# Optimization experiments

Measured on AMD Instinct MI355X. Metric: run time of the kernel, lower is better.

The kernel has to match this reference:

```python
import jax, jax.numpy as jnp
import numpy as np

N_HEAD = 8
D_HEAD = 64  # emb_size == d_model // n_head


def _proj(x, w):
    # x: (B, 1, d_model, max_len), w: (n_head*emb_size, 1, 25, 1) -> conv VALID
    y = jax.lax.conv_general_dilated(
        x, w, window_strides=(1, 1), padding='VALID',
        dimension_numbers=('NCHW', 'OIHW', 'NCHW'))  # (B, C, H1, L)
    B, C, H1, L = y.shape
    y = y.reshape(B, C, H1 // N_HEAD, N_HEAD, L).mean(axis=3)  # (B, C, H2, L)
    # view(B, -1, n_head, d_head).transpose(1, 2) -> (B, n_head, S, d_head)
    y = y.reshape(B, -1, N_HEAD, D_HEAD).transpose(0, 2, 1, 3)
    return y


def setup_inputs() -> dict:
    key = jax.random.key(0)
    ks = jax.random.split(key, 7)
    B, d_model, max_len = 8, 512, 16
    C = N_HEAD * D_HEAD  # 512
    return {
        'query': jax.random.normal(ks[0], (B, 1, d_model, max_len), jnp.float32),
        'key':   jax.random.normal(ks[1], (B, 1, d_model, max_len), jnp.float32),
        'value': jax.random.normal(ks[2], (B, 1, d_model, max_len), jnp.float32),
        'wq': jax.random.normal(ks[3], (C, 1, 25, 1), jnp.float32) * 0.1,
        'wk': jax.random.normal(ks[4], (C, 1, 25, 1), jnp.float32) * 0.1,
        'wv': jax.random.normal(ks[5], (C, 1, 25, 1), jnp.float32) * 0.1,
        'w_out': jax.random.normal(ks[6], (1, 1, 1, 1), jnp.float32),
        'b_out': jnp.zeros((1,), jnp.float32),
    }


def reference(query, key, value, wq, wk, wv, w_out, b_out):
    q = _proj(query, wq)   # (B, H, S, Dh)
    k = _proj(key, wk)
    v = _proj(value, wv)
    scale = 1.0 / jnp.sqrt(jnp.asarray(D_HEAD, q.dtype))
    scores = jnp.einsum('bhqd,bhkd->bhqk', q, k) * scale
    attn = jax.nn.softmax(scores, axis=-1)  # dropout is identity in eval
    x = jnp.einsum('bhqk,bhkd->bhqd', attn, v)
    B = x.shape[0]
    x = x.transpose(0, 2, 1, 3).reshape(B, -1, N_HEAD * D_HEAD)  # (B, S, d_model)
    # conv_out: 1x1 Conv2d(1,1) == scalar scale + bias
    x = x * w_out.reshape(()) + b_out.reshape(())
    return x, attn
```

## Files before the change

kernel.cpp:

```cpp
#include <hip/hip_runtime.h>
#include <hip/hip_bf16.h>
#include <cstdint>
#include <cstddef>

#define B_    8
#define H_    8
#define BH_   64
#define S_    976
#define SP_   992
#define D_    64
#define DM_   512
#define L_    16
#define H2_   61
#define KW_   25
#define EFF_  32
#define XOFF  3997696
#define OSTR  68
#define PWC   132

typedef __attribute__((ext_vector_type(8))) short bf16x8;
typedef __attribute__((ext_vector_type(4))) short bf16x4;
typedef __attribute__((ext_vector_type(4))) unsigned short u16x4;
typedef __attribute__((ext_vector_type(4))) float f32x4;

__device__ __forceinline__ unsigned short f2bfu(float f) {
    union { float f; unsigned u; } v; v.f = f;
    unsigned u = v.u;
    u += 0x7fffu + ((u >> 16) & 1u);
    return (unsigned short)(u >> 16);
}
__device__ __forceinline__ unsigned packbf(float a, float b) {
    return (unsigned)f2bfu(a) | ((unsigned)f2bfu(b) << 16);
}
__device__ __forceinline__ float bflo(unsigned u) {
    union { unsigned u; float f; } v; v.u = u << 16; return v.f;
}
__device__ __forceinline__ float bfhi(unsigned u) {
    union { unsigned u; float f; } v; v.u = u & 0xffff0000u; return v.f;
}

__device__ __forceinline__ f32x4 mfma16(bf16x4 a, bf16x4 b, f32x4 c) {
#if __has_builtin(__builtin_amdgcn_mfma_f32_16x16x16bf16_1k)
    return __builtin_amdgcn_mfma_f32_16x16x16bf16_1k(a, b, c, 0, 0, 0);
#else
    asm volatile("v_mfma_f32_16x16x16_bf16 %0, %1, %2, %0"
                 : "+v"(c) : "v"(a), "v"(b));
    return c;
#endif
}

__global__ __launch_bounds__(256) void proj_kernel(
    const float* __restrict__ qin, const float* __restrict__ kin,
    const float* __restrict__ vin, const float* __restrict__ wq,
    const float* __restrict__ wk, const float* __restrict__ wv,
    short* __restrict__ qws, short* __restrict__ kws, short* __restrict__ vtws) {
    __shared__ float xl[536 * L_];
    __shared__ float wl[32 * 32];
    int blk = blockIdx.x;
    int cg  = blk & 15;
    int b   = (blk >> 4) & 7;
    int tz  = blk >> 7;
    const float* x    = (tz == 0) ? qin : (tz == 1) ? kin : vin;
    const float* wsrc = (tz == 0) ? wq  : (tz == 1) ? wk  : wv;

    const float4* xb4 = (const float4*)(x + b * DM_ * L_);
    float4* xl4 = (float4*)xl;
    for (int i = threadIdx.x; i < DM_ * L_ / 4; i += 256) xl4[i] = xb4[i];
    for (int i = DM_ * L_ + threadIdx.x; i < 536 * L_; i += 256) xl[i] = 0.f;

    for (int i = threadIdx.x; i < 1024; i += 256) {
        int ci = i >> 5;
        int t  = i & 31;
        int c  = cg * 32 + ci;
        int jlo = (t - 24 > 0) ? t - 24 : 0;
        int jhi = (t < 7) ? t : 7;
        float s = 0.f;
        for (int jj = jlo; jj <= jhi; ++jj) s += wsrc[c * KW_ + (t - jj)];
        wl[i] = s * 0.125f;
    }
    __syncthreads();

    int c_local = threadIdx.x >> 3;
    int slot    = threadIdx.x & 7;
    int c       = cg * 32 + c_local;
    float wreg[EFF_];
    #pragma unroll
    for (int i = 0; i < EFF_; ++i) wreg[i] = wl[c_local * 32 + i];

    for (int it = 0; it < 8; ++it) {
        int pt  = slot + it * 8;
        int h2b = pt >> 2;
        int l0  = (pt & 3) * 4;
        float acc[4][4];
        #pragma unroll
        for (int d = 0; d < 4; ++d)
            #pragma unroll
            for (int jj = 0; jj < 4; ++jj) acc[d][jj] = 0.f;
        const float* xp = &xl[(h2b * 32) * L_ + l0];
        #pragma unroll
        for (int k = 0; k < 56; ++k) {
            float4 xv = *(const float4*)(xp + k * L_);
            #pragma unroll
            for (int d = 0; d < 4; ++d) {
                int t = k - 8 * d;
                if (t >= 0 && t < EFF_) {
                    acc[d][0] = fmaf(xv.x, wreg[t], acc[d][0]);
                    acc[d][1] = fmaf(xv.y, wreg[t], acc[d][1]);
                    acc[d][2] = fmaf(xv.z, wreg[t], acc[d][2]);
                    acc[d][3] = fmaf(xv.w, wreg[t], acc[d][3]);
                }
            }
        }
        #pragma unroll
        for (int d = 0; d < 4; ++d) {
            int h2 = h2b * 4 + d;
            if (h2 < H2_) {
                int f0   = c * S_ + h2 * L_ + l0;
                int s    = f0 >> 9;
                int head = (f0 >> 6) & 7;
                int dh   = f0 & 63;
                int bh   = b * H_ + head;
                if (tz == 2) {
                    #pragma unroll
                    for (int jj = 0; jj < 4; ++jj)
                        vtws[((size_t)bh * D_ + dh + jj) * SP_ + s] =
                            (short)f2bfu(acc[d][jj]);
                } else {
                    u16x4 u = { f2bfu(acc[d][0]), f2bfu(acc[d][1]),
                                f2bfu(acc[d][2]), f2bfu(acc[d][3]) };
                    short* dst = (tz == 0) ? qws : kws;
                    *(u16x4*)(void*)&dst[((size_t)bh * S_ + s) * D_ + dh] = u;
                }
            }
        }
    }
}

__global__ __launch_bounds__(256) void attn_kernel(
    const short* __restrict__ qws, const short* __restrict__ kws,
    const short* __restrict__ vtws, const float* __restrict__ w_out,
    const float* __restrict__ b_out, float* __restrict__ out) {
    __shared__ unsigned pw[4][16][PWC];
    __shared__ float sums[4][16];

    int w    = threadIdx.x >> 6;
    int lane = threadIdx.x & 63;
    int l16  = lane & 15;
    int g    = lane >> 4;

    int blk = blockIdx.x;
    int xcd = blk & 7;
    int j   = blk >> 3;
    int bh  = xcd + 8 * (j / H2_);
    int qt  = j % H2_;
    int s0  = qt * 16;

    int t0 = (w == 0) ? 0 : 16 + (w - 1) * 15;
    int nt = (w == 0) ? 16 : 15;

    const short* qb = qws + ((size_t)bh * S_ + s0 + l16) * D_ + g * 8;
    bf16x8 q0 = *(const bf16x8*)qb;
    bf16x8 q1 = *(const bf16x8*)(qb + 32);
    const short* kbase = kws + ((size_t)bh * S_ + l16) * D_ + g * 8;
    const short* vbase = vtws + ((size_t)bh * D_ + l16) * SP_ + g * 4;

    f32x4 o0 = {0.f,0.f,0.f,0.f}, o1 = {0.f,0.f,0.f,0.f};
    f32x4 o2 = {0.f,0.f,0.f,0.f}, o3 = {0.f,0.f,0.f,0.f};
    float sa = 0.f, sb = 0.f, sc_ = 0.f, sd = 0.f;

    #pragma unroll
    for (int ct = 0; ct < 16; ++ct) {
        if (ct < nt) {
            int gt = t0 + ct;
            const short* kb = kbase + (size_t)gt * 16 * D_;
            bf16x8 k0 = *(const bf16x8*)kb;
            bf16x8 k1 = *(const bf16x8*)(kb + 32);
            const short* vb = vbase + gt * 16;
            bf16x4 v0 = *(const bf16x4*)(vb);
            bf16x4 v1 = *(const bf16x4*)(vb + 16 * SP_);
            bf16x4 v2 = *(const bf16x4*)(vb + 32 * SP_);
            bf16x4 v3 = *(const bf16x4*)(vb + 48 * SP_);
            f32x4 acc = {0.f, 0.f, 0.f, 0.f};
            acc = __builtin_amdgcn_mfma_f32_16x16x32_bf16(k0, q0, acc, 0, 0, 0);
            acc = __builtin_amdgcn_mfma_f32_16x16x32_bf16(k1, q1, acc, 0, 0, 0);
            float e0 = __expf(acc[0] * 0.125f);
            float e1 = __expf(acc[1] * 0.125f);
            float e2 = __expf(acc[2] * 0.125f);
            float e3 = __expf(acc[3] * 0.125f);
            sa += e0; sb += e1; sc_ += e2; sd += e3;
            unsigned u0 = packbf(e0, e1);
            unsigned u1 = packbf(e2, e3);
            uint2 pk2 = {u0, u1};
            *(uint2*)(void*)&pw[w][l16][ct * 8 + g * 2] = pk2;
            union { uint2 u; bf16x4 v; } pc;
            pc.u.x = u0; pc.u.y = u1;
            o0 = mfma16(pc.v, v0, o0);
            o1 = mfma16(pc.v, v1, o1);
            o2 = mfma16(pc.v, v2, o2);
            o3 = mfma16(pc.v, v3, o3);
        }
    }
    float sum = (sa + sb) + (sc_ + sd);
    sum += __shfl_xor(sum, 16);
    sum += __shfl_xor(sum, 32);
    if (lane < 16) sums[w][l16] = sum;
    __syncthreads();

    {
        int colbase = t0 * 16;
        bool act = lane < nt * 4;
        float* abase = out + XOFF + ((size_t)bh * S_ + s0) * S_ + colbase + lane * 4;
        #pragma unroll
        for (int r = 0; r < 16; ++r) {
            float invr = 1.f / ((sums[0][r] + sums[1][r]) +
                                (sums[2][r] + sums[3][r]));
            if (act) {
                uint2 raw = *(const uint2*)(void*)&pw[w][r][lane * 2];
                f32x4 pv = { bflo(raw.x) * invr, bfhi(raw.x) * invr,
                             bflo(raw.y) * invr, bfhi(raw.y) * invr };
                __builtin_nontemporal_store(pv, (f32x4*)(abase + (size_t)r * S_));
            }
        }
    }
    __syncthreads();

    float* olds = (float*)&pw[0][0][0];
    {
        float* ob = olds + w * 16 * OSTR;
        #pragma unroll
        for (int i = 0; i < 4; ++i) {
            int q = g * 4 + i;
            ob[q * OSTR +  0 + l16] = o0[i];
            ob[q * OSTR + 16 + l16] = o1[i];
            ob[q * OSTR + 32 + l16] = o2[i];
            ob[q * OSTR + 48 + l16] = o3[i];
        }
    }
    __syncthreads();

    {
        float wo = w_out[0], bo = b_out[0];
        int b = bh >> 3, hh = bh & 7;
        #pragma unroll
        for (int rr = 0; rr < 4; ++rr) {
            int r = w * 4 + rr;
            float invr = 1.f / ((sums[0][r] + sums[1][r]) +
                                (sums[2][r] + sums[3][r]));
            float s1 = invr * wo;
            int o = r * OSTR + lane;
            float v = olds[o] + olds[16*OSTR + o] + olds[32*OSTR + o] +
                      olds[48*OSTR + o];
            out[((size_t)b * S_ + s0 + r) * DM_ + hh * D_ + lane] = v * s1 + bo;
        }
    }
}

extern "C" void kernel_launch(void* const* d_in, const int* in_sizes, int n_in,
                              void* d_out, int out_size, void* d_ws, size_t ws_size,
                              hipStream_t stream) {
    const float* q   = (const float*)d_in[0];
    const float* k   = (const float*)d_in[1];
    const float* v   = (const float*)d_in[2];
    const float* wq  = (const float*)d_in[3];
    const float* wk  = (const float*)d_in[4];
    const float* wv  = (const float*)d_in[5];
    const float* wo  = (const float*)d_in[6];
    const float* bo  = (const float*)d_in[7];

    char* ws = (char*)d_ws;
    short* qws  = (short*)(ws + 196608);
    short* kws  = qws + (size_t)BH_ * S_ * D_;
    short* vtws = kws + (size_t)BH_ * S_ * D_;

    proj_kernel<<<384, 256, 0, stream>>>(q, k, v, wq, wk, wv, qws, kws, vtws);
    attn_kernel<<<BH_ * H2_, 256, 0, stream>>>(qws, kws, vtws, wo, bo,
                                               (float*)d_out);
}
```

Before: 176.3 us.

## Store attention tile as flat contiguous block with shared reciprocal row sums

```diff
diff --git a/kernel.cpp b/kernel.cpp
--- a/kernel.cpp
+++ b/kernel.cpp
@@ -16,7 +16,8 @@
 #define EFF_  32
 #define XOFF  3997696
 #define OSTR  68
-#define PWC   132
+#define PWR   492
+#define TFL   15616
 
 typedef __attribute__((ext_vector_type(8))) short bf16x8;
 typedef __attribute__((ext_vector_type(4))) short bf16x4;
@@ -140,8 +141,9 @@
     const short* __restrict__ qws, const short* __restrict__ kws,
     const short* __restrict__ vtws, const float* __restrict__ w_out,
     const float* __restrict__ b_out, float* __restrict__ out) {
-    __shared__ unsigned pw[4][16][PWC];
+    __shared__ unsigned pw[16][PWR];
     __shared__ float sums[4][16];
+    __shared__ float inv16[16];
 
     int w    = threadIdx.x >> 6;
     int lane = threadIdx.x & 63;
@@ -191,7 +193,7 @@
             unsigned u0 = packbf(e0, e1);
             unsigned u1 = packbf(e2, e3);
             uint2 pk2 = {u0, u1};
-            *(uint2*)(void*)&pw[w][l16][ct * 8 + g * 2] = pk2;
+            *(uint2*)(void*)&pw[l16][gt * 8 + g * 2] = pk2;
             union { uint2 u; bf16x4 v; } pc;
             pc.u.x = u0; pc.u.y = u1;
             o0 = mfma16(pc.v, v0, o0);
@@ -206,25 +208,33 @@
     if (lane < 16) sums[w][l16] = sum;
     __syncthreads();
 
+    if (threadIdx.x < 16) {
+        int r = threadIdx.x;
+        inv16[r] = 1.f / ((sums[0][r] + sums[1][r]) +
+                          (sums[2][r] + sums[3][r]));
+    }
+    __syncthreads();
+
     {
-        int colbase = t0 * 16;
-        bool act = lane < nt * 4;
-        float* abase = out + XOFF + ((size_t)bh * S_ + s0) * S_ + colbase + lane * 4;
-        #pragma unroll
-        for (int r = 0; r < 16; ++r) {
-            float invr = 1.f / ((sums[0][r] + sums[1][r]) +
-                                (sums[2][r] + sums[3][r]));
-            if (act) {
-                uint2 raw = *(const uint2*)(void*)&pw[w][r][lane * 2];
+        float* tbase = out + XOFF + ((size_t)bh * S_ + s0) * S_;
+        int base = w * 256 + lane * 4;
+        #pragma unroll
+        for (int rd = 0; rd < 16; ++rd) {
+            int ff = rd * 1024 + base;
+            if (ff < TFL) {
+                int r = ((ff >> 4) * 2149) >> 17;
+                int c = ff - 976 * r;
+                uint2 raw = *(const uint2*)(void*)&pw[r][c >> 1];
+                float invr = inv16[r];
                 f32x4 pv = { bflo(raw.x) * invr, bfhi(raw.x) * invr,
                              bflo(raw.y) * invr, bfhi(raw.y) * invr };
-                __builtin_nontemporal_store(pv, (f32x4*)(abase + (size_t)r * S_));
+                *(f32x4*)(tbase + ff) = pv;
             }
         }
     }
     __syncthreads();
 
-    float* olds = (float*)&pw[0][0][0];
+    float* olds = (float*)&pw[0][0];
     {
         float* ob = olds + w * 16 * OSTR;
         #pragma unroll
@@ -244,9 +254,7 @@
         #pragma unroll
         for (int rr = 0; rr < 4; ++rr) {
             int r = w * 4 + rr;
-            float invr = 1.f / ((sums[0][r] + sums[1][r]) +
-                                (sums[2][r] + sums[3][r]));
-            float s1 = invr * wo;
+            float s1 = inv16[r] * wo;
             int o = r * OSTR + lane;
             float v = olds[o] + olds[16*OSTR + o] + olds[32*OSTR + o] +
                       olds[48*OSTR + o];
```

New measurement: 178.0 us. Within noise of the previous version (+1.0%).
